# Optimization experiments

Hardware: AMD Instinct MI355X
Metric: run time of the kernel (lower is better)

The kernel has to match this reference:

```python
import jax, jax.numpy as jnp
import numpy as np

B, C, H, W = 2, 128, 128, 128
K, STRIDE, DIL, NH = 8, 2, 2, 8
HID = int(C * 4 / 3)  # 170


def _ln(x, g, b):
    # layernorm2d: normalize over channel axis (last axis in NHWC)
    mu = jnp.mean(x, axis=-1, keepdims=True)
    xc = x - mu
    var = jnp.mean(xc * xc, axis=-1, keepdims=True)
    return xc * jax.lax.rsqrt(var + 1e-6) * g + b


def _nat_attn(xn, qkv_w, qkv_b, qg, qb, kg, kb, proj_w, proj_b):
    # dilated/strided local-neighborhood attention (NATTEN-style)
    Bq, Hq, Wq, Cq = xn.shape
    dh = Cq // NH
    qkv = xn @ qkv_w.T + qkv_b
    q, k, v = jnp.split(qkv, 3, axis=-1)
    q = _ln(q, qg, qb)
    k = _ln(k, kg, kb)
    # keys/values on a stride-subsampled grid
    kc = k[:, ::STRIDE, ::STRIDE, :]
    vc = v[:, ::STRIDE, ::STRIDE, :]
    Hc, Wc = Hq // STRIDE, Wq // STRIDE
    plo = DIL * (K // 2)
    phi = DIL * (K - 1 - K // 2)
    pad = ((0, 0), (plo, phi), (plo, phi), (0, 0))
    kp = jnp.pad(kc, pad)
    vp = jnp.pad(vc, pad)
    mp = jnp.pad(jnp.ones((1, Hc, Wc, 1), dtype=bool), pad)
    offs = [(i * DIL, j * DIL) for i in range(K) for j in range(K)]  # fixed k*k window taps
    kn = jnp.stack([kp[:, a:a + Hc, b:b + Wc, :] for a, b in offs], axis=3).reshape(Bq, Hc, Wc, K * K, NH, dh)
    vn = jnp.stack([vp[:, a:a + Hc, b:b + Wc, :] for a, b in offs], axis=3).reshape(Bq, Hc, Wc, K * K, NH, dh)
    mn = jnp.stack([mp[:, a:a + Hc, b:b + Wc, 0] for a, b in offs], axis=3)  # [1,Hc,Wc,kk]
    # each full-res query maps to its coarse kv cell: [B,Hc,stride,Wc,stride,heads,dh]
    q6 = q.reshape(Bq, Hc, STRIDE, Wc, STRIDE, NH, dh)
    scores = jnp.einsum('bisjtnd,bijknd->bisjtnk', q6, kn) * (dh ** -0.5)
    m = mn[:, :, None, :, None, None, :]
    scores = jnp.where(m, scores, jnp.float32(-1e30))
    attn = jax.nn.softmax(scores, axis=-1)
    out = jnp.einsum('bisjtnk,bijknd->bisjtnd', attn, vn).reshape(Bq, Hq, Wq, Cq)
    return out @ proj_w.T + proj_b


def _cffn(xn, fc1_w, fc1_b, mg, mb, fc2_w, fc2_b):
    h = xn @ fc1_w.T + fc1_b
    h = _ln(h, mg, mb)
    h = jax.nn.gelu(h, approximate=True)  # gelu_tanh
    return h @ fc2_w.T + fc2_b


def setup_inputs():
    key = jax.random.key(0)
    ks = jax.random.split(key, 6)
    w = lambda k, shp: jax.random.normal(k, shp, dtype=jnp.float32) * 0.02
    z = lambda n: jnp.zeros((n,), jnp.float32)
    o = lambda n: jnp.ones((n,), jnp.float32)
    return {
        'x': jax.random.normal(ks[0], (B, C, H, W), dtype=jnp.float32),
        'qkv_w': w(ks[1], (3 * C, C)), 'qkv_b': z(3 * C),
        'qg': o(C), 'qb': z(C), 'kg': o(C), 'kb': z(C),
        'proj_w': w(ks[2], (C, C)), 'proj_b': z(C),
        'n1g': o(C), 'n1b': z(C), 'n2g': o(C), 'n2b': z(C),
        'ls1_g': jnp.full((C,), 1e-5, jnp.float32),
        'ls2_g': jnp.full((C,), 1e-5, jnp.float32),
        'fc1_w': w(ks[3], (HID, C)), 'fc1_b': z(HID),
        'mg': o(HID), 'mb': z(HID),
        'fc2_w': w(ks[4], (C, HID)), 'fc2_b': z(C),
    }


def reference(x, qkv_w, qkv_b, qg, qb, kg, kb, proj_w, proj_b, n1g, n1b, n2g, n2b, ls1_g, ls2_g, fc1_w, fc1_b, mg, mb, fc2_w, fc2_b):
    xh = jnp.transpose(x, (0, 2, 3, 1))  # NCHW -> NHWC
    xh = xh + ls1_g * _nat_attn(_ln(xh, n1g, n1b), qkv_w, qkv_b, qg, qb, kg, kb, proj_w, proj_b)
    xh = xh + ls2_g * _cffn(_ln(xh, n2g, n2b), fc1_w, fc1_b, mg, mb, fc2_w, fc2_b)
    return jnp.transpose(xh, (0, 3, 1, 2))
```

## Files before the change

### kernel.cpp

```cpp
#include <hip/hip_runtime.h>
#include <hip/hip_bf16.h>

typedef __hip_bfloat16 BF;
typedef __attribute__((ext_vector_type(8))) short bf16x8;
typedef __attribute__((ext_vector_type(4))) float f32x4;


#define ASTR 200
#define KSTR 136

__device__ __forceinline__ void gsum8(float v[8], float* red){
  #pragma unroll
  for(int s = 1; s < 64; s <<= 1){
    #pragma unroll
    for(int i = 0; i < 8; i++) v[i] += __shfl_xor(v[i], s);
  }
  const int wid = threadIdx.x >> 6;
  __syncthreads();
  if((threadIdx.x & 63) == 0){
    #pragma unroll
    for(int i = 0; i < 8; i++) red[wid*8 + i] = v[i];
  }
  __syncthreads();
  #pragma unroll
  for(int i = 0; i < 8; i++) v[i] = red[i] + red[8 + i];
}

__device__ __forceinline__ void rowred(float s1[4], float s2[4], float* red,
                                       int wave, int lane){
  #pragma unroll
  for(int m = 1; m < 16; m <<= 1){
    #pragma unroll
    for(int r = 0; r < 4; r++){ s1[r] += __shfl_xor(s1[r], m); s2[r] += __shfl_xor(s2[r], m); }
  }
  const int q4 = lane >> 4;
  __syncthreads();
  if((lane & 15) == 0){
    #pragma unroll
    for(int r = 0; r < 4; r++){
      red[wave*32 + q4*4 + r]      = s1[r];
      red[wave*32 + 16 + q4*4 + r] = s2[r];
    }
  }
  __syncthreads();
  #pragma unroll
  for(int r = 0; r < 4; r++){
    s1[r] = red[q4*4 + r]      + red[32 + q4*4 + r];
    s2[r] = red[16 + q4*4 + r] + red[48 + q4*4 + r];
  }
}

__global__ void k_tin(const float* __restrict__ x, float* __restrict__ xt){
  __shared__ float tile[32][33];
  const int b = blockIdx.z;
  const int pb = blockIdx.x * 32;
  const int cb = blockIdx.y * 32;
  const int tx = threadIdx.x, ty = threadIdx.y;
  #pragma unroll
  for(int r = 0; r < 32; r += 8)
    tile[ty+r][tx] = x[(size_t)(b*128 + cb+ty+r)*16384 + pb + tx];
  __syncthreads();
  #pragma unroll
  for(int r = 0; r < 32; r += 8)
    xt[(size_t)((b<<14) + pb + ty + r)*128 + cb + tx] = tile[tx][ty+r];
}

__global__ void k_wt(const float* __restrict__ qkv_w, const float* __restrict__ proj_w,
                     const float* __restrict__ fc1_w, const float* __restrict__ fc2_w,
                     BF* __restrict__ pk){
  const int idx = blockIdx.x * 256 + threadIdx.x;
  if(idx >= 112640) return;
  float val;
  if(idx < 49152){
    const int reg = idx >> 14, l = idx & 16383;
    const int j = l & 7, q = (l>>3)&3, n = (l>>5)&127, s = l>>12;
    val = qkv_w[(reg*128 + n)*128 + (s*32 + q*8 + j)];
  } else if(idx < 65536){
    const int l = idx - 49152;
    const int j = l&7, q=(l>>3)&3, n=(l>>5)&127, s=l>>12;
    val = proj_w[n*128 + (s*32+q*8+j)];
  } else if(idx < 88064){
    const int l = idx - 65536;
    const int j = l&7, q=(l>>3)&3, rem = l>>5;
    const int n = rem % 176, s = rem / 176;
    const int k = s*32+q*8+j;
    val = (n < 170) ? fc1_w[n*128 + k] : 0.f;
  } else {
    const int l = idx - 88064;
    const int j = l&7, q=(l>>3)&3, n=(l>>5)&127, s=l>>12;
    const int k = s*32+q*8+j;
    val = (k < 170) ? fc2_w[n*170 + k] : 0.f;
  }
  pk[idx] = __float2bfloat16(val);
}

__global__ void __launch_bounds__(128)
k_kv(const float* __restrict__ xt,
     const BF* __restrict__ packK, const BF* __restrict__ packV,
     const float* __restrict__ qkv_b,
     const float* __restrict__ kg, const float* __restrict__ kb,
     const float* __restrict__ n1g, const float* __restrict__ n1b,
     float* __restrict__ kcb, float* __restrict__ vcb){
  __shared__ BF Abuf[16*KSTR];
  __shared__ float red[64];
  const int tid = threadIdx.x, wave = tid>>6, lane = tid&63;
  const int l15 = lane & 15, q4 = lane >> 4;
  const int bx = blockIdx.x;
  size_t prow[8];
  float xv[8];
  #pragma unroll
  for(int r = 0; r < 8; r++){
    const int cp = bx*8 + r;
    const int b = cp>>12, rm = cp&4095, ic = rm>>6, jcc = rm&63;
    prow[r] = ((size_t)(b*16384 + (2*ic)*128 + 2*jcc))*128;
    xv[r] = xt[prow[r] + tid];
  }
  float v[8];
  #pragma unroll
  for(int r = 0; r < 8; r++) v[r] = xv[r];
  gsum8(v, red);
  float xc[8], sq[8];
  #pragma unroll
  for(int r = 0; r < 8; r++){ xc[r] = xv[r] - v[r]*(1.f/128.f); sq[r] = xc[r]*xc[r]; }
  gsum8(sq, red);
  {
    const float g = n1g[tid], be = n1b[tid];
    #pragma unroll
    for(int r = 0; r < 8; r++)
      Abuf[r*KSTR + tid] = __float2bfloat16(xc[r]*rsqrtf(sq[r]*(1.f/128.f)+1e-6f)*g + be);
  }
  __syncthreads();
  bf16x8 af[4];
  #pragma unroll
  for(int s = 0; s < 4; s++) af[s] = *(const bf16x8*)&Abuf[l15*KSTR + s*32 + q4*8];

  f32x4 acc[4];
  #pragma unroll
  for(int nt = 0; nt < 4; nt++){ acc[nt][0]=0.f; acc[nt][1]=0.f; acc[nt][2]=0.f; acc[nt][3]=0.f; }
  #pragma unroll
  for(int nt = 0; nt < 4; nt++){
    const int n = (wave*4+nt)*16 + l15;
    #pragma unroll
    for(int s = 0; s < 4; s++){
      bf16x8 bf = *(const bf16x8*)&packK[((s*128 + n)*4 + q4)*8];
      acc[nt] = __builtin_amdgcn_mfma_f32_16x16x32_bf16(af[s], bf, acc[nt], 0,0,0);
    }
  }
  float s1[4], s2[4], colb[4];
  #pragma unroll
  for(int r = 0; r < 4; r++){ s1[r]=0.f; s2[r]=0.f; }
  #pragma unroll
  for(int nt = 0; nt < 4; nt++){
    colb[nt] = qkv_b[128 + (wave*4+nt)*16 + l15];
    #pragma unroll
    for(int r = 0; r < 4; r++){
      const float vv = acc[nt][r] + colb[nt];
      acc[nt][r] = vv; s1[r] += vv; s2[r] += vv*vv;
    }
  }
  rowred(s1, s2, red, wave, lane);
  #pragma unroll
  for(int nt = 0; nt < 4; nt++){
    const int col = (wave*4+nt)*16 + l15;
    const float g = kg[col], be = kb[col];
    #pragma unroll
    for(int r = 0; r < 4; r++){
      const int row = q4*4 + r;
      if(row < 8){
        const float mu = s1[r]*(1.f/128.f);
        const float var = s2[r]*(1.f/128.f) - mu*mu;
        kcb[(size_t)(bx*8+row)*128 + col] = (acc[nt][r]-mu)*rsqrtf(var+1e-6f)*g + be;
      }
    }
  }
  #pragma unroll
  for(int nt = 0; nt < 4; nt++){ acc[nt][0]=0.f; acc[nt][1]=0.f; acc[nt][2]=0.f; acc[nt][3]=0.f; }
  #pragma unroll
  for(int nt = 0; nt < 4; nt++){
    const int n = (wave*4+nt)*16 + l15;
    #pragma unroll
    for(int s = 0; s < 4; s++){
      bf16x8 bf = *(const bf16x8*)&packV[((s*128 + n)*4 + q4)*8];
      acc[nt] = __builtin_amdgcn_mfma_f32_16x16x32_bf16(af[s], bf, acc[nt], 0,0,0);
    }
  }
  #pragma unroll
  for(int nt = 0; nt < 4; nt++){
    const int col = (wave*4+nt)*16 + l15;
    const float bv = qkv_b[256 + col];
    #pragma unroll
    for(int r = 0; r < 4; r++){
      const int row = q4*4 + r;
      if(row < 8) vcb[(size_t)(bx*8+row)*128 + col] = acc[nt][r] + bv;
    }
  }
}

__global__ void __launch_bounds__(128, 4)
k_cell(const float* __restrict__ xt_in,
       const BF* __restrict__ packQ, const BF* __restrict__ packP,
       const BF* __restrict__ packF1, const BF* __restrict__ packF2,
       const float* __restrict__ qkv_b,
       const float* __restrict__ qg, const float* __restrict__ qb,
       const float* __restrict__ n1g, const float* __restrict__ n1b,
       const float* __restrict__ proj_b,
       const float* __restrict__ ls1, const float* __restrict__ ls2,
       const float* __restrict__ n2g, const float* __restrict__ n2b,
       const float* __restrict__ fc1_b,
       const float* __restrict__ mg, const float* __restrict__ mb,
       const float* __restrict__ fc2_b,
       const float* __restrict__ kcb, const float* __restrict__ vcb,
       float* __restrict__ xt_out){
  __shared__ float4 uni[512];
  BF* const Abuf = (BF*)uni;
  float4* const sc4 = uni;
  __shared__ float xvL[8*128];
  __shared__ float4 qnA[128], qnB[128];
  __shared__ int cidxA[64], cidxB[64];
  __shared__ float red[64];
  const int tid = threadIdx.x, wave = tid>>6, lane = tid&63;
  const int l15 = lane & 15, q4 = lane >> 4;

  const int bx = blockIdx.x;
  const int b = bx >> 11, rem = bx & 2047, ip = rem >> 6, jc = rem & 63;
  const int icA = 2*ip, icB = 2*ip + 1;
  const size_t p0 = (size_t)b*16384*128 + ((size_t)(4*ip)*128 + 2*jc)*128;
  float xv[8];
  #pragma unroll
  for(int r = 0; r < 8; r++){
    const size_t pr = p0 + ((size_t)(r>>1)<<14) + (size_t)((r&1)<<7);
    xv[r] = xt_in[pr + tid]; xvL[r*128 + tid] = xv[r];
  }

  float v[8];
  #pragma unroll
  for(int r = 0; r < 8; r++) v[r] = xv[r];
  gsum8(v, red);
  float xc[8], sq[8];
  #pragma unroll
  for(int r = 0; r < 8; r++){ xc[r] = xv[r] - v[r]*(1.f/128.f); sq[r] = xc[r]*xc[r]; }
  gsum8(sq, red);
  {
    const float g = n1g[tid], be = n1b[tid];
    #pragma unroll
    for(int r = 0; r < 8; r++)
      Abuf[r*ASTR + tid] = __float2bfloat16(xc[r]*rsqrtf(sq[r]*(1.f/128.f)+1e-6f)*g + be);
  }
  if(tid < 64){
    const int i = tid >> 3, j = tid & 7;
    const int rj = jc + 2*j - 8;
    const bool vj = (rj >= 0) && (rj < 64);
    const int riA = icA + 2*i - 8, riB = icB + 2*i - 8;
    cidxA[tid] = (vj && riA >= 0 && riA < 64) ? ((b*4096 + riA*64 + rj)*128) : 0;
    cidxB[tid] = (vj && riB >= 0 && riB < 64) ? ((b*4096 + riB*64 + rj)*128) : 0;
  }
  __syncthreads();

  {
    bf16x8 af[4];
    #pragma unroll
    for(int s = 0; s < 4; s++) af[s] = *(const bf16x8*)&Abuf[l15*ASTR + s*32 + q4*8];
    f32x4 acc[4];
    #pragma unroll
    for(int nt = 0; nt < 4; nt++){ acc[nt][0]=0.f; acc[nt][1]=0.f; acc[nt][2]=0.f; acc[nt][3]=0.f; }
    #pragma unroll
    for(int nt = 0; nt < 4; nt++){
      const int n = (wave*4+nt)*16 + l15;
      #pragma unroll
      for(int s = 0; s < 4; s++){
        bf16x8 bf = *(const bf16x8*)&packQ[((s*128 + n)*4 + q4)*8];
        acc[nt] = __builtin_amdgcn_mfma_f32_16x16x32_bf16(af[s], bf, acc[nt], 0,0,0);
      }
    }
    float s1[4], s2[4];
    #pragma unroll
    for(int r = 0; r < 4; r++){ s1[r]=0.f; s2[r]=0.f; }
    #pragma unroll
    for(int nt = 0; nt < 4; nt++){
      const float cb2 = qkv_b[(wave*4+nt)*16 + l15];
      #pragma unroll
      for(int r = 0; r < 4; r++){
        const float vv = acc[nt][r] + cb2;
        acc[nt][r] = vv; s1[r] += vv; s2[r] += vv*vv;
      }
    }
    rowred(s1, s2, red, wave, lane);
    if(q4 < 2){
      float mu[4], rs[4];
      #pragma unroll
      for(int r = 0; r < 4; r++){
        mu[r] = s1[r]*(1.f/128.f);
        rs[r] = rsqrtf(s2[r]*(1.f/128.f) - mu[r]*mu[r] + 1e-6f);
      }
      #pragma unroll
      for(int nt = 0; nt < 4; nt++){
        const int col = (wave*4+nt)*16 + l15;
        const float g = qg[col], be = qb[col];
        float4 t;
        t.x = (acc[nt][0]-mu[0])*rs[0]*g + be;
        t.y = (acc[nt][1]-mu[1])*rs[1]*g + be;
        t.z = (acc[nt][2]-mu[2])*rs[2]*g + be;
        t.w = (acc[nt][3]-mu[3])*rs[3]*g + be;
        if(q4 == 0) qnA[col] = t; else qnB[col] = t;
      }
    }
  }
  __syncthreads();

  const int i8 = lane >> 3, j8 = lane & 7;
  const int rjm = jc + 2*j8 - 8;
  const bool vjm = (rjm >= 0) && (rjm < 64);
  const int riAm = icA + 2*i8 - 8, riBm = icB + 2*i8 - 8;
  const float maddA = (vjm && riAm >= 0 && riAm < 64) ? 0.f : -1e30f;
  const float maddB = (vjm && riBm >= 0 && riBm < 64) ? 0.f : -1e30f;

  float4 oA, oB;
  for(int cell = 0; cell < 2; cell++){
    const int* cidx = cell ? cidxB : cidxA;
    const float4* qn = cell ? qnB : qnA;
    const float madd = cell ? maddB : maddA;
    {
      const int ci = cidx[lane];
      float4 kf[4][4];
      #pragma unroll
      for(int rep = 0; rep < 4; rep++){
        const int n = rep*2 + wave;
        const float4* kp4 = (const float4*)(kcb + (size_t)ci + n*16);
        #pragma unroll
        for(int d4 = 0; d4 < 4; d4++) kf[rep][d4] = kp4[d4];
      }
      #pragma unroll
      for(int rep = 0; rep < 4; rep++){
        const int n = rep*2 + wave;
        float4 a; a.x = 0.f; a.y = 0.f; a.z = 0.f; a.w = 0.f;
        #pragma unroll
        for(int d4 = 0; d4 < 4; d4++){
          const float4 kv = kf[rep][d4];
          #pragma unroll
          for(int e = 0; e < 4; e++){
            const float4 qq = qn[n*16 + d4*4 + e];
            const float kd = (e==0) ? kv.x : (e==1) ? kv.y : (e==2) ? kv.z : kv.w;
            a.x += qq.x*kd; a.y += qq.y*kd; a.z += qq.z*kd; a.w += qq.w*kd;
          }
        }
        float4 s;
        s.x = a.x*0.25f + madd; s.y = a.y*0.25f + madd;
        s.z = a.z*0.25f + madd; s.w = a.w*0.25f + madd;
        sc4[rep*128 + tid] = s;
      }
    }
    __syncthreads();
    {
      const int n = tid >> 4, l = tid & 15;
      float4 s0 = sc4[n*64 + l], s1 = sc4[n*64 + l + 16];
      float4 s2 = sc4[n*64 + l + 32], s3 = sc4[n*64 + l + 48];
      float4 m;
      m.x = fmaxf(fmaxf(s0.x,s1.x), fmaxf(s2.x,s3.x));
      m.y = fmaxf(fmaxf(s0.y,s1.y), fmaxf(s2.y,s3.y));
      m.z = fmaxf(fmaxf(s0.z,s1.z), fmaxf(s2.z,s3.z));
      m.w = fmaxf(fmaxf(s0.w,s1.w), fmaxf(s2.w,s3.w));
      #pragma unroll
      for(int sft = 1; sft < 16; sft <<= 1){
        m.x = fmaxf(m.x, __shfl_xor(m.x, sft));
        m.y = fmaxf(m.y, __shfl_xor(m.y, sft));
        m.z = fmaxf(m.z, __shfl_xor(m.z, sft));
        m.w = fmaxf(m.w, __shfl_xor(m.w, sft));
      }
      float4 e0, e1, e2, e3, es;
      e0.x = __expf(s0.x-m.x); e0.y = __expf(s0.y-m.y); e0.z = __expf(s0.z-m.z); e0.w = __expf(s0.w-m.w);
      e1.x = __expf(s1.x-m.x); e1.y = __expf(s1.y-m.y); e1.z = __expf(s1.z-m.z); e1.w = __expf(s1.w-m.w);
      e2.x = __expf(s2.x-m.x); e2.y = __expf(s2.y-m.y); e2.z = __expf(s2.z-m.z); e2.w = __expf(s2.w-m.w);
      e3.x = __expf(s3.x-m.x); e3.y = __expf(s3.y-m.y); e3.z = __expf(s3.z-m.z); e3.w = __expf(s3.w-m.w);
      es.x = e0.x+e1.x+e2.x+e3.x; es.y = e0.y+e1.y+e2.y+e3.y;
      es.z = e0.z+e1.z+e2.z+e3.z; es.w = e0.w+e1.w+e2.w+e3.w;
      #pragma unroll
      for(int sft = 1; sft < 16; sft <<= 1){
        es.x += __shfl_xor(es.x, sft); es.y += __shfl_xor(es.y, sft);
        es.z += __shfl_xor(es.z, sft); es.w += __shfl_xor(es.w, sft);
      }
      float4 inv; inv.x = 1.f/es.x; inv.y = 1.f/es.y; inv.z = 1.f/es.z; inv.w = 1.f/es.w;
      float4 o;
      o.x = e0.x*inv.x; o.y = e0.y*inv.y; o.z = e0.z*inv.z; o.w = e0.w*inv.w; sc4[n*64+l]    = o;
      o.x = e1.x*inv.x; o.y = e1.y*inv.y; o.z = e1.z*inv.z; o.w = e1.w*inv.w; sc4[n*64+l+16] = o;
      o.x = e2.x*inv.x; o.y = e2.y*inv.y; o.z = e2.z*inv.z; o.w = e2.w*inv.w; sc4[n*64+l+32] = o;
      o.x = e3.x*inv.x; o.y = e3.y*inv.y; o.z = e3.z*inv.z; o.w = e3.w*inv.w; sc4[n*64+l+48] = o;
    }
    __syncthreads();
    {
      const int n = tid >> 4;
      float4 o; o.x = 0.f; o.y = 0.f; o.z = 0.f; o.w = 0.f;
      #pragma unroll 2
      for(int nb0 = 0; nb0 < 64; nb0 += 8){
        float vv[8];
        #pragma unroll
        for(int u = 0; u < 8; u++) vv[u] = vcb[(size_t)cidx[nb0+u] + tid];
        #pragma unroll
        for(int u = 0; u < 8; u++){
          const float4 pr = sc4[n*64 + nb0 + u];
          o.x += pr.x*vv[u]; o.y += pr.y*vv[u]; o.z += pr.z*vv[u]; o.w += pr.w*vv[u];
        }
      }
      if(cell == 0) oA = o; else oB = o;
    }
    __syncthreads();
  }
  Abuf[0*ASTR + tid] = __float2bfloat16(oA.x);
  Abuf[1*ASTR + tid] = __float2bfloat16(oA.y);
  Abuf[2*ASTR + tid] = __float2bfloat16(oA.z);
  Abuf[3*ASTR + tid] = __float2bfloat16(oA.w);
  Abuf[4*ASTR + tid] = __float2bfloat16(oB.x);
  Abuf[5*ASTR + tid] = __float2bfloat16(oB.y);
  Abuf[6*ASTR + tid] = __float2bfloat16(oB.z);
  Abuf[7*ASTR + tid] = __float2bfloat16(oB.w);
  __syncthreads();

  float xh[4][4];
  {
    bf16x8 af[4];
    #pragma unroll
    for(int s = 0; s < 4; s++) af[s] = *(const bf16x8*)&Abuf[l15*ASTR + s*32 + q4*8];
    f32x4 acc[4];
    #pragma unroll
    for(int nt = 0; nt < 4; nt++){ acc[nt][0]=0.f; acc[nt][1]=0.f; acc[nt][2]=0.f; acc[nt][3]=0.f; }
    #pragma unroll
    for(int nt = 0; nt < 4; nt++){
      const int n = (wave*4+nt)*16 + l15;
      #pragma unroll
      for(int s = 0; s < 4; s++){
        bf16x8 bf = *(const bf16x8*)&packP[((s*128 + n)*4 + q4)*8];
        acc[nt] = __builtin_amdgcn_mfma_f32_16x16x32_bf16(af[s], bf, acc[nt], 0,0,0);
      }
    }
    float s1[4], s2[4];
    #pragma unroll
    for(int r = 0; r < 4; r++){ s1[r]=0.f; s2[r]=0.f; }
    #pragma unroll
    for(int nt = 0; nt < 4; nt++){
      const int col = (wave*4+nt)*16 + l15;
      const float bp = proj_b[col], l1 = ls1[col];
      #pragma unroll
      for(int r = 0; r < 4; r++){
        const int row = q4*4 + r;
        const float xvv = (row < 8) ? xvL[row*128 + col] : 0.f;
        const float hx = xvv + l1*(acc[nt][r] + bp);
        xh[nt][r] = hx; s1[r] += hx; s2[r] += hx*hx;
      }
    }
    rowred(s1, s2, red, wave, lane);
    #pragma unroll
    for(int nt = 0; nt < 4; nt++){
      const int col = (wave*4+nt)*16 + l15;
      const float g = n2g[col], be = n2b[col];
      #pragma unroll
      for(int r = 0; r < 4; r++){
        const int row = q4*4 + r;
        if(row < 8){
          const float mu = s1[r]*(1.f/128.f);
          const float var = s2[r]*(1.f/128.f) - mu*mu;
          Abuf[row*ASTR + col] =
            __float2bfloat16((xh[nt][r]-mu)*rsqrtf(var+1e-6f)*g + be);
        }
      }
    }
  }
  __syncthreads();

  {
    bf16x8 af[4];
    #pragma unroll
    for(int s = 0; s < 4; s++) af[s] = *(const bf16x8*)&Abuf[l15*ASTR + s*32 + q4*8];
    const int NT1 = wave ? 5 : 6;
    f32x4 acc1[6];
    #pragma unroll
    for(int nt = 0; nt < 6; nt++){ acc1[nt][0]=0.f; acc1[nt][1]=0.f; acc1[nt][2]=0.f; acc1[nt][3]=0.f; }
    for(int nt = 0; nt < NT1; nt++){
      const int tI = wave ? (6 + nt) : nt;
      const int n = tI*16 + l15;
      #pragma unroll
      for(int s = 0; s < 4; s++){
        bf16x8 bf = *(const bf16x8*)&packF1[((s*176 + n)*4 + q4)*8];
        acc1[nt] = __builtin_amdgcn_mfma_f32_16x16x32_bf16(af[s], bf, acc1[nt], 0,0,0);
      }
    }
    float s1[4], s2[4];
    #pragma unroll
    for(int r = 0; r < 4; r++){ s1[r]=0.f; s2[r]=0.f; }
    for(int nt = 0; nt < NT1; nt++){
      const int tI = wave ? (6 + nt) : nt;
      const int col = tI*16 + l15;
      const float b1 = (col < 170) ? fc1_b[col] : 0.f;
      #pragma unroll
      for(int r = 0; r < 4; r++){
        const float vv = acc1[nt][r] + b1;
        acc1[nt][r] = vv; s1[r] += vv; s2[r] += vv*vv;
      }
    }
    rowred(s1, s2, red, wave, lane);
    for(int z = tid; z < 176; z += 128){
      const int row = z / 22, col = 170 + (z - (z/22)*22);
      Abuf[row*ASTR + col] = __float2bfloat16(0.f);
    }
    const float kA = 0.7978845608028654f, kB = 0.044715f;
    for(int nt = 0; nt < NT1; nt++){
      const int tI = wave ? (6 + nt) : nt;
      const int col = tI*16 + l15;
      if(col < 170){
        const float g = mg[col], be = mb[col];
        #pragma unroll
        for(int r = 0; r < 4; r++){
          const int row = q4*4 + r;
          if(row < 8){
            const float mu = s1[r]*(1.f/170.f);
            const float var = s2[r]*(1.f/170.f) - mu*mu;
            const float hn = (acc1[nt][r]-mu)*rsqrtf(var+1e-6f)*g + be;
            const float gl = 0.5f*hn*(1.f + tanhf(kA*(hn + kB*hn*hn*hn)));
            Abuf[row*ASTR + col] = __float2bfloat16(gl);
          }
        }
      }
    }
  }
  __syncthreads();

  {
    bf16x8 af[6];
    #pragma unroll
    for(int s = 0; s < 6; s++) af[s] = *(const bf16x8*)&Abuf[l15*ASTR + s*32 + q4*8];
    f32x4 acc[4];
    #pragma unroll
    for(int nt = 0; nt < 4; nt++){ acc[nt][0]=0.f; acc[nt][1]=0.f; acc[nt][2]=0.f; acc[nt][3]=0.f; }
    #pragma unroll
    for(int nt = 0; nt < 4; nt++){
      const int n = (wave*4+nt)*16 + l15;
      #pragma unroll
      for(int s = 0; s < 6; s++){
        bf16x8 bf = *(const bf16x8*)&packF2[((s*128 + n)*4 + q4)*8];
        acc[nt] = __builtin_amdgcn_mfma_f32_16x16x32_bf16(af[s], bf, acc[nt], 0,0,0);
      }
    }
    #pragma unroll
    for(int nt = 0; nt < 4; nt++){
      const int col = (wave*4+nt)*16 + l15;
      const float bf2 = fc2_b[col], l2 = ls2[col];
      #pragma unroll
      for(int r = 0; r < 4; r++){
        const int row = q4*4 + r;
        if(row < 8)
          xt_out[p0 + ((size_t)(row>>1)<<14) + (size_t)((row&1)<<7) + col] =
            xh[nt][r] + l2*(acc[nt][r] + bf2);
      }
    }
  }
}

__global__ void k_tout(const float* __restrict__ xt, float* __restrict__ out){
  __shared__ float tile[32][33];
  const int b = blockIdx.z;
  const int pb = blockIdx.x * 32;
  const int cb = blockIdx.y * 32;
  const int tx = threadIdx.x, ty = threadIdx.y;
  #pragma unroll
  for(int r = 0; r < 32; r += 8)
    tile[ty+r][tx] = xt[(size_t)((b<<14) + pb + ty + r)*128 + cb + tx];
  __syncthreads();
  #pragma unroll
  for(int r = 0; r < 32; r += 8)
    out[(size_t)(b*128 + cb + ty + r)*16384 + pb + tx] = tile[tx][ty+r];
}

extern "C" void kernel_launch(void* const* d_in, const int* in_sizes, int n_in,
                              void* d_out, int out_size, void* d_ws, size_t ws_size,
                              hipStream_t stream){
  const float* x      = (const float*)d_in[0];
  const float* qkv_w  = (const float*)d_in[1];
  const float* qkv_b  = (const float*)d_in[2];
  const float* qg     = (const float*)d_in[3];
  const float* qb     = (const float*)d_in[4];
  const float* kg     = (const float*)d_in[5];
  const float* kb     = (const float*)d_in[6];
  const float* proj_w = (const float*)d_in[7];
  const float* proj_b = (const float*)d_in[8];
  const float* n1g    = (const float*)d_in[9];
  const float* n1b    = (const float*)d_in[10];
  const float* n2g    = (const float*)d_in[11];
  const float* n2b    = (const float*)d_in[12];
  const float* ls1    = (const float*)d_in[13];
  const float* ls2    = (const float*)d_in[14];
  const float* fc1_w  = (const float*)d_in[15];
  const float* fc1_b  = (const float*)d_in[16];
  const float* mg     = (const float*)d_in[17];
  const float* mb     = (const float*)d_in[18];
  const float* fc2_w  = (const float*)d_in[19];
  const float* fc2_b  = (const float*)d_in[20];

  float* ws  = (float*)d_ws;
  float* xt  = ws;
  float* kcb = ws + 4194304;
  float* vcb = ws + 5242880;
  BF* pk     = (BF*)(ws + 6291456);
  BF* packQ  = pk;
  BF* packK  = pk + 16384;
  BF* packV  = pk + 32768;
  BF* packP  = pk + 49152;
  BF* packF1 = pk + 65536;
  BF* packF2 = pk + 88064;

  dim3 tgrid(512, 4, 2), tblk(32, 8);
  k_tin <<<tgrid, tblk, 0, stream>>>(x, xt);
  k_wt  <<<440, 256, 0, stream>>>(qkv_w, proj_w, fc1_w, fc2_w, pk);
  k_kv  <<<1024, 128, 0, stream>>>(xt, packK, packV, qkv_b, kg, kb, n1g, n1b, kcb, vcb);
  k_cell<<<4096, 128, 0, stream>>>(xt, packQ, packP, packF1, packF2,
                                   qkv_b, qg, qb, n1g, n1b, proj_b, ls1, ls2,
                                   n2g, n2b, fc1_b, mg, mb, fc2_b,
                                   kcb, vcb, xt);
  k_tout<<<tgrid, tblk, 0, stream>>>(xt, (float*)d_out);
}
```

Baseline: 235.7 us.

## Move neighborhood attention QK and PV onto bf16 MFMA with per-wave head groups

```diff
diff --git a/kernel.cpp b/kernel.cpp
--- a/kernel.cpp
+++ b/kernel.cpp
@@ -9,21 +9,33 @@
 #define ASTR 200
 #define KSTR 136
 
-__device__ __forceinline__ void gsum8(float v[8], float* red){
+__device__ __forceinline__ short bfr(float f){
+  union{float f; unsigned u;} c; c.f = f;
+  const unsigned u = c.u + 0x7FFFu + ((c.u >> 16) & 1u);
+  return (short)(u >> 16);
+}
+__device__ __forceinline__ bf16x8 pk8(float4 a, float4 b){
+  bf16x8 r;
+  r[0]=bfr(a.x); r[1]=bfr(a.y); r[2]=bfr(a.z); r[3]=bfr(a.w);
+  r[4]=bfr(b.x); r[5]=bfr(b.y); r[6]=bfr(b.z); r[7]=bfr(b.w);
+  return r;
+}
+
+__device__ __forceinline__ void gsum16(float v[16], float* red){
   #pragma unroll
   for(int s = 1; s < 64; s <<= 1){
     #pragma unroll
-    for(int i = 0; i < 8; i++) v[i] += __shfl_xor(v[i], s);
+    for(int i = 0; i < 16; i++) v[i] += __shfl_xor(v[i], s);
   }
   const int wid = threadIdx.x >> 6;
   __syncthreads();
   if((threadIdx.x & 63) == 0){
     #pragma unroll
-    for(int i = 0; i < 8; i++) red[wid*8 + i] = v[i];
-  }
-  __syncthreads();
-  #pragma unroll
-  for(int i = 0; i < 8; i++) v[i] = red[i] + red[8 + i];
+    for(int i = 0; i < 16; i++) red[wid*16 + i] = v[i];
+  }
+  __syncthreads();
+  #pragma unroll
+  for(int i = 0; i < 16; i++) v[i] = red[i] + red[16 + i];
 }
 
 __device__ __forceinline__ void rowred(float s1[4], float s2[4], float* red,
@@ -106,28 +118,25 @@
   const int tid = threadIdx.x, wave = tid>>6, lane = tid&63;
   const int l15 = lane & 15, q4 = lane >> 4;
   const int bx = blockIdx.x;
-  size_t prow[8];
   float xv[8];
   #pragma unroll
   for(int r = 0; r < 8; r++){
     const int cp = bx*8 + r;
     const int b = cp>>12, rm = cp&4095, ic = rm>>6, jcc = rm&63;
-    prow[r] = ((size_t)(b*16384 + (2*ic)*128 + 2*jcc))*128;
-    xv[r] = xt[prow[r] + tid];
-  }
-  float v[8];
-  #pragma unroll
-  for(int r = 0; r < 8; r++) v[r] = xv[r];
-  gsum8(v, red);
-  float xc[8], sq[8];
-  #pragma unroll
-  for(int r = 0; r < 8; r++){ xc[r] = xv[r] - v[r]*(1.f/128.f); sq[r] = xc[r]*xc[r]; }
-  gsum8(sq, red);
+    xv[r] = xt[((size_t)(b*16384 + (2*ic)*128 + 2*jcc))*128 + tid];
+  }
+  float st[16];
+  #pragma unroll
+  for(int r = 0; r < 8; r++){ st[r] = xv[r]; st[8+r] = xv[r]*xv[r]; }
+  gsum16(st, red);
   {
     const float g = n1g[tid], be = n1b[tid];
     #pragma unroll
-    for(int r = 0; r < 8; r++)
-      Abuf[r*KSTR + tid] = __float2bfloat16(xc[r]*rsqrtf(sq[r]*(1.f/128.f)+1e-6f)*g + be);
+    for(int r = 0; r < 8; r++){
+      const float mu = st[r]*(1.f/128.f);
+      const float var = st[8+r]*(1.f/128.f) - mu*mu;
+      Abuf[r*KSTR + tid] = __float2bfloat16((xv[r]-mu)*rsqrtf(var+1e-6f)*g + be);
+    }
   }
   __syncthreads();
   bf16x8 af[4];
@@ -146,15 +155,15 @@
       acc[nt] = __builtin_amdgcn_mfma_f32_16x16x32_bf16(af[s], bf, acc[nt], 0,0,0);
     }
   }
-  float s1[4], s2[4], colb[4];
+  float s1[4], s2[4];
   #pragma unroll
   for(int r = 0; r < 4; r++){ s1[r]=0.f; s2[r]=0.f; }
   #pragma unroll
   for(int nt = 0; nt < 4; nt++){
-    colb[nt] = qkv_b[128 + (wave*4+nt)*16 + l15];
+    const float colb = qkv_b[128 + (wave*4+nt)*16 + l15];
     #pragma unroll
     for(int r = 0; r < 4; r++){
-      const float vv = acc[nt][r] + colb[nt];
+      const float vv = acc[nt][r] + colb;
       acc[nt][r] = vv; s1[r] += vv; s2[r] += vv*vv;
     }
   }
@@ -211,11 +220,10 @@
        const float* __restrict__ fc2_b,
        const float* __restrict__ kcb, const float* __restrict__ vcb,
        float* __restrict__ xt_out){
-  __shared__ float4 uni[512];
-  BF* const Abuf = (BF*)uni;
-  float4* const sc4 = uni;
+  __shared__ __align__(16) BF uni[6912];
+  BF* const Abuf = uni;
   __shared__ float xvL[8*128];
-  __shared__ float4 qnA[128], qnB[128];
+  __shared__ float4 qnA[136], qnB[136];
   __shared__ int cidxA[64], cidxB[64];
   __shared__ float red[64];
   const int tid = threadIdx.x, wave = tid>>6, lane = tid&63;
@@ -232,27 +240,26 @@
     xv[r] = xt_in[pr + tid]; xvL[r*128 + tid] = xv[r];
   }
 
-  float v[8];
-  #pragma unroll
-  for(int r = 0; r < 8; r++) v[r] = xv[r];
-  gsum8(v, red);
-  float xc[8], sq[8];
-  #pragma unroll
-  for(int r = 0; r < 8; r++){ xc[r] = xv[r] - v[r]*(1.f/128.f); sq[r] = xc[r]*xc[r]; }
-  gsum8(sq, red);
+  float st[16];
+  #pragma unroll
+  for(int r = 0; r < 8; r++){ st[r] = xv[r]; st[8+r] = xv[r]*xv[r]; }
+  gsum16(st, red);
   {
     const float g = n1g[tid], be = n1b[tid];
     #pragma unroll
-    for(int r = 0; r < 8; r++)
-      Abuf[r*ASTR + tid] = __float2bfloat16(xc[r]*rsqrtf(sq[r]*(1.f/128.f)+1e-6f)*g + be);
+    for(int r = 0; r < 8; r++){
+      const float mu = st[r]*(1.f/128.f);
+      const float var = st[8+r]*(1.f/128.f) - mu*mu;
+      Abuf[r*ASTR + tid] = __float2bfloat16((xv[r]-mu)*rsqrtf(var+1e-6f)*g + be);
+    }
   }
   if(tid < 64){
     const int i = tid >> 3, j = tid & 7;
-    const int rj = jc + 2*j - 8;
-    const bool vj = (rj >= 0) && (rj < 64);
+    const int rj0 = jc + 2*j - 8;
+    const bool vj0 = (rj0 >= 0) && (rj0 < 64);
     const int riA = icA + 2*i - 8, riB = icB + 2*i - 8;
-    cidxA[tid] = (vj && riA >= 0 && riA < 64) ? ((b*4096 + riA*64 + rj)*128) : 0;
-    cidxB[tid] = (vj && riB >= 0 && riB < 64) ? ((b*4096 + riB*64 + rj)*128) : 0;
+    cidxA[tid] = (vj0 && riA >= 0 && riA < 64) ? ((b*4096 + riA*64 + rj0)*128) : 0;
+    cidxB[tid] = (vj0 && riB >= 0 && riB < 64) ? ((b*4096 + riB*64 + rj0)*128) : 0;
   }
   __syncthreads();
 
@@ -301,117 +308,128 @@
         t.y = (acc[nt][1]-mu[1])*rs[1]*g + be;
         t.z = (acc[nt][2]-mu[2])*rs[2]*g + be;
         t.w = (acc[nt][3]-mu[3])*rs[3]*g + be;
-        if(q4 == 0) qnA[col] = t; else qnB[col] = t;
-      }
-    }
-  }
-  __syncthreads();
-
-  const int i8 = lane >> 3, j8 = lane & 7;
-  const int rjm = jc + 2*j8 - 8;
-  const bool vjm = (rjm >= 0) && (rjm < 64);
-  const int riAm = icA + 2*i8 - 8, riBm = icB + 2*i8 - 8;
-  const float maddA = (vjm && riAm >= 0 && riAm < 64) ? 0.f : -1e30f;
-  const float maddB = (vjm && riBm >= 0 && riBm < 64) ? 0.f : -1e30f;
-
-  float4 oA, oB;
+        const int pidx = col + (wave*4+nt);
+        if(q4 == 0) qnA[pidx] = t; else qnB[pidx] = t;
+      }
+    }
+  }
+  __syncthreads();
+
+  const int g = wave;
+  const int hsub = l15 >> 2, px = l15 & 3;
+  const int par = q4 >> 1, dbase = (q4 & 1) * 8;
+  BF* const attw = uni + wave*3456;
+  ushort* const Vt = (ushort*)attw;
+  ushort* const Pb = (ushort*)(attw + 2304);
+  const int i0 = l15 >> 3;
+  const int rj = jc + 2*(l15 & 7) - 8;
+  const bool vj = (rj >= 0) && (rj < 64);
+
+  f32x4 oC[2];
+  #pragma unroll
   for(int cell = 0; cell < 2; cell++){
     const int* cidx = cell ? cidxB : cidxA;
-    const float4* qn = cell ? qnB : qnA;
-    const float madd = cell ? maddB : maddA;
+    const float* qf = (const float*)(cell ? qnB : qnA);
+    const int ic = cell ? icB : icA;
+    float madd[4];
+    #pragma unroll
+    for(int nt = 0; nt < 4; nt++){
+      const int ri = ic + 2*(nt*2 + i0) - 8;
+      madd[nt] = (vj && ri >= 0 && ri < 64) ? 0.f : -1e30f;
+    }
+    bf16x8 afq0, afq1;
     {
-      const int ci = cidx[lane];
-      float4 kf[4][4];
-      #pragma unroll
-      for(int rep = 0; rep < 4; rep++){
-        const int n = rep*2 + wave;
-        const float4* kp4 = (const float4*)(kcb + (size_t)ci + n*16);
+      const int fidx = (g*64 + hsub*16 + dbase + (g*4 + hsub))*4 + px;
+      short bq[8];
+      #pragma unroll
+      for(int j = 0; j < 8; j++) bq[j] = bfr(qf[fidx + 4*j]);
+      const bool a0 = (par == hsub), a1 = ((2 + par) == hsub);
+      #pragma unroll
+      for(int j = 0; j < 8; j++){
+        afq0[j] = a0 ? bq[j] : (short)0;
+        afq1[j] = a1 ? bq[j] : (short)0;
+      }
+    }
+    f32x4 accq[4];
+    #pragma unroll
+    for(int nt = 0; nt < 4; nt++){ accq[nt][0]=0.f; accq[nt][1]=0.f; accq[nt][2]=0.f; accq[nt][3]=0.f; }
+    #pragma unroll
+    for(int nt = 0; nt < 4; nt++){
+      const float* kp = kcb + (size_t)cidx[nt*16 + l15] + g*64 + q4*8;
+      const float4 k00 = *(const float4*)kp;
+      const float4 k01 = *(const float4*)(kp + 4);
+      const float4 k10 = *(const float4*)(kp + 32);
+      const float4 k11 = *(const float4*)(kp + 36);
+      accq[nt] = __builtin_amdgcn_mfma_f32_16x16x32_bf16(afq0, pk8(k00,k01), accq[nt], 0,0,0);
+      accq[nt] = __builtin_amdgcn_mfma_f32_16x16x32_bf16(afq1, pk8(k10,k11), accq[nt], 0,0,0);
+    }
+    float inv[4];
+    #pragma unroll
+    for(int reg = 0; reg < 4; reg++){
+      const float s0 = accq[0][reg]*0.25f + madd[0];
+      const float s1 = accq[1][reg]*0.25f + madd[1];
+      const float s2 = accq[2][reg]*0.25f + madd[2];
+      const float s3 = accq[3][reg]*0.25f + madd[3];
+      float m = fmaxf(fmaxf(s0,s1), fmaxf(s2,s3));
+      #pragma unroll
+      for(int sft = 1; sft < 16; sft <<= 1) m = fmaxf(m, __shfl_xor(m, sft));
+      const float e0 = __expf(s0-m), e1 = __expf(s1-m);
+      const float e2 = __expf(s2-m), e3 = __expf(s3-m);
+      ushort* pr = Pb + (q4*4 + reg)*72 + l15;
+      pr[0]  = (ushort)bfr(e0);
+      pr[16] = (ushort)bfr(e1);
+      pr[32] = (ushort)bfr(e2);
+      pr[48] = (ushort)bfr(e3);
+      float es = e0+e1+e2+e3;
+      #pragma unroll
+      for(int sft = 1; sft < 16; sft <<= 1) es += __shfl_xor(es, sft);
+      inv[reg] = 1.f/es;
+    }
+    const bf16x8 pa0 = *(const bf16x8*)(Pb + l15*72 + q4*8);
+    const bf16x8 pa1 = *(const bf16x8*)(Pb + l15*72 + 32 + q4*8);
+
+    f32x4 oSel; oSel[0]=0.f; oSel[1]=0.f; oSel[2]=0.f; oSel[3]=0.f;
+    #pragma unroll
+    for(int pr2 = 0; pr2 < 2; pr2++){
+      #pragma unroll
+      for(int sl = 0; sl < 2; sl++){
+        const int h = g*4 + pr2*2 + sl;
         #pragma unroll
-        for(int d4 = 0; d4 < 4; d4++) kf[rep][d4] = kp4[d4];
-      }
-      #pragma unroll
-      for(int rep = 0; rep < 4; rep++){
-        const int n = rep*2 + wave;
-        float4 a; a.x = 0.f; a.y = 0.f; a.z = 0.f; a.w = 0.f;
-        #pragma unroll
-        for(int d4 = 0; d4 < 4; d4++){
-          const float4 kv = kf[rep][d4];
-          #pragma unroll
-          for(int e = 0; e < 4; e++){
-            const float4 qq = qn[n*16 + d4*4 + e];
-            const float kd = (e==0) ? kv.x : (e==1) ? kv.y : (e==2) ? kv.z : kv.w;
-            a.x += qq.x*kd; a.y += qq.y*kd; a.z += qq.z*kd; a.w += qq.w*kd;
-          }
+        for(int it = 0; it < 4; it++){
+          const int nb = l15*4 + it;
+          const float4 vv = *(const float4*)(vcb + (size_t)cidx[nb] + h*16 + q4*4);
+          ushort* wp = Vt + sl*1152 + (q4*4)*72 + nb;
+          wp[0]    = (ushort)bfr(vv.x);
+          wp[72]   = (ushort)bfr(vv.y);
+          wp[144]  = (ushort)bfr(vv.z);
+          wp[216]  = (ushort)bfr(vv.w);
         }
-        float4 s;
-        s.x = a.x*0.25f + madd; s.y = a.y*0.25f + madd;
-        s.z = a.z*0.25f + madd; s.w = a.w*0.25f + madd;
-        sc4[rep*128 + tid] = s;
-      }
-    }
-    __syncthreads();
-    {
-      const int n = tid >> 4, l = tid & 15;
-      float4 s0 = sc4[n*64 + l], s1 = sc4[n*64 + l + 16];
-      float4 s2 = sc4[n*64 + l + 32], s3 = sc4[n*64 + l + 48];
-      float4 m;
-      m.x = fmaxf(fmaxf(s0.x,s1.x), fmaxf(s2.x,s3.x));
-      m.y = fmaxf(fmaxf(s0.y,s1.y), fmaxf(s2.y,s3.y));
-      m.z = fmaxf(fmaxf(s0.z,s1.z), fmaxf(s2.z,s3.z));
-      m.w = fmaxf(fmaxf(s0.w,s1.w), fmaxf(s2.w,s3.w));
-      #pragma unroll
-      for(int sft = 1; sft < 16; sft <<= 1){
-        m.x = fmaxf(m.x, __shfl_xor(m.x, sft));
-        m.y = fmaxf(m.y, __shfl_xor(m.y, sft));
-        m.z = fmaxf(m.z, __shfl_xor(m.z, sft));
-        m.w = fmaxf(m.w, __shfl_xor(m.w, sft));
-      }
-      float4 e0, e1, e2, e3, es;
-      e0.x = __expf(s0.x-m.x); e0.y = __expf(s0.y-m.y); e0.z = __expf(s0.z-m.z); e0.w = __expf(s0.w-m.w);
-      e1.x = __expf(s1.x-m.x); e1.y = __expf(s1.y-m.y); e1.z = __expf(s1.z-m.z); e1.w = __expf(s1.w-m.w);
-      e2.x = __expf(s2.x-m.x); e2.y = __expf(s2.y-m.y); e2.z = __expf(s2.z-m.z); e2.w = __expf(s2.w-m.w);
-      e3.x = __expf(s3.x-m.x); e3.y = __expf(s3.y-m.y); e3.z = __expf(s3.z-m.z); e3.w = __expf(s3.w-m.w);
-      es.x = e0.x+e1.x+e2.x+e3.x; es.y = e0.y+e1.y+e2.y+e3.y;
-      es.z = e0.z+e1.z+e2.z+e3.z; es.w = e0.w+e1.w+e2.w+e3.w;
-      #pragma unroll
-      for(int sft = 1; sft < 16; sft <<= 1){
-        es.x += __shfl_xor(es.x, sft); es.y += __shfl_xor(es.y, sft);
-        es.z += __shfl_xor(es.z, sft); es.w += __shfl_xor(es.w, sft);
-      }
-      float4 inv; inv.x = 1.f/es.x; inv.y = 1.f/es.y; inv.z = 1.f/es.z; inv.w = 1.f/es.w;
-      float4 o;
-      o.x = e0.x*inv.x; o.y = e0.y*inv.y; o.z = e0.z*inv.z; o.w = e0.w*inv.w; sc4[n*64+l]    = o;
-      o.x = e1.x*inv.x; o.y = e1.y*inv.y; o.z = e1.z*inv.z; o.w = e1.w*inv.w; sc4[n*64+l+16] = o;
-      o.x = e2.x*inv.x; o.y = e2.y*inv.y; o.z = e2.z*inv.z; o.w = e2.w*inv.w; sc4[n*64+l+32] = o;
-      o.x = e3.x*inv.x; o.y = e3.y*inv.y; o.z = e3.z*inv.z; o.w = e3.w*inv.w; sc4[n*64+l+48] = o;
-    }
-    __syncthreads();
-    {
-      const int n = tid >> 4;
-      float4 o; o.x = 0.f; o.y = 0.f; o.z = 0.f; o.w = 0.f;
-      #pragma unroll 2
-      for(int nb0 = 0; nb0 < 64; nb0 += 8){
-        float vv[8];
-        #pragma unroll
-        for(int u = 0; u < 8; u++) vv[u] = vcb[(size_t)cidx[nb0+u] + tid];
-        #pragma unroll
-        for(int u = 0; u < 8; u++){
-          const float4 pr = sc4[n*64 + nb0 + u];
-          o.x += pr.x*vv[u]; o.y += pr.y*vv[u]; o.z += pr.z*vv[u]; o.w += pr.w*vv[u];
-        }
-      }
-      if(cell == 0) oA = o; else oB = o;
-    }
-    __syncthreads();
-  }
-  Abuf[0*ASTR + tid] = __float2bfloat16(oA.x);
-  Abuf[1*ASTR + tid] = __float2bfloat16(oA.y);
-  Abuf[2*ASTR + tid] = __float2bfloat16(oA.z);
-  Abuf[3*ASTR + tid] = __float2bfloat16(oA.w);
-  Abuf[4*ASTR + tid] = __float2bfloat16(oB.x);
-  Abuf[5*ASTR + tid] = __float2bfloat16(oB.y);
-  Abuf[6*ASTR + tid] = __float2bfloat16(oB.z);
-  Abuf[7*ASTR + tid] = __float2bfloat16(oB.w);
+      }
+      #pragma unroll
+      for(int sl = 0; sl < 2; sl++){
+        const int hs = pr2*2 + sl;
+        const bf16x8 bv0 = *(const bf16x8*)(Vt + sl*1152 + l15*72 + q4*8);
+        const bf16x8 bv1 = *(const bf16x8*)(Vt + sl*1152 + l15*72 + 32 + q4*8);
+        f32x4 accv; accv[0]=0.f; accv[1]=0.f; accv[2]=0.f; accv[3]=0.f;
+        accv = __builtin_amdgcn_mfma_f32_16x16x32_bf16(pa0, bv0, accv, 0,0,0);
+        accv = __builtin_amdgcn_mfma_f32_16x16x32_bf16(pa1, bv1, accv, 0,0,0);
+        if(q4 == hs){ oSel[0]=accv[0]; oSel[1]=accv[1]; oSel[2]=accv[2]; oSel[3]=accv[3]; }
+      }
+    }
+    oC[cell][0] = oSel[0]*inv[0]; oC[cell][1] = oSel[1]*inv[1];
+    oC[cell][2] = oSel[2]*inv[2]; oC[cell][3] = oSel[3]*inv[3];
+  }
+  __syncthreads();
+  {
+    const int col = (g*4 + q4)*16 + l15;
+    ushort* ab = (ushort*)Abuf;
+    #pragma unroll
+    for(int cell = 0; cell < 2; cell++){
+      #pragma unroll
+      for(int reg = 0; reg < 4; reg++)
+        ab[(cell*4 + reg)*ASTR + col] = (ushort)bfr(oC[cell][reg]);
+    }
+  }
   __syncthreads();
 
   float xh[4][4];
@@ -450,7 +468,7 @@
     #pragma unroll
     for(int nt = 0; nt < 4; nt++){
       const int col = (wave*4+nt)*16 + l15;
-      const float g = n2g[col], be = n2b[col];
+      const float g2 = n2g[col], be = n2b[col];
       #pragma unroll
       for(int r = 0; r < 4; r++){
         const int row = q4*4 + r;
@@ -458,7 +476,7 @@
           const float mu = s1[r]*(1.f/128.f);
           const float var = s2[r]*(1.f/128.f) - mu*mu;
           Abuf[row*ASTR + col] =
-            __float2bfloat16((xh[nt][r]-mu)*rsqrtf(var+1e-6f)*g + be);
+            __float2bfloat16((xh[nt][r]-mu)*rsqrtf(var+1e-6f)*g2 + be);
         }
       }
     }
@@ -505,15 +523,16 @@
       const int tI = wave ? (6 + nt) : nt;
       const int col = tI*16 + l15;
       if(col < 170){
-        const float g = mg[col], be = mb[col];
+        const float g2 = mg[col], be = mb[col];
         #pragma unroll
         for(int r = 0; r < 4; r++){
           const int row = q4*4 + r;
           if(row < 8){
             const float mu = s1[r]*(1.f/170.f);
             const float var = s2[r]*(1.f/170.f) - mu*mu;
-            const float hn = (acc1[nt][r]-mu)*rsqrtf(var+1e-6f)*g + be;
-            const float gl = 0.5f*hn*(1.f + tanhf(kA*(hn + kB*hn*hn*hn)));
+            const float hn = (acc1[nt][r]-mu)*rsqrtf(var+1e-6f)*g2 + be;
+            const float u = kA*(hn + kB*hn*hn*hn);
+            const float gl = hn / (1.f + __expf(-2.f*u));
             Abuf[row*ASTR + col] = __float2bfloat16(gl);
           }
         }
```

Result: slower. 256.6 us (+8.9%).
